# Kernel optimization log

Hardware: AMD Instinct MI355X
Metric: run time of the kernel (lower is better)

The kernel has to match this reference:

```python
import jax, jax.numpy as jnp
import numpy as np

N, M, D, E, G = 2048, 1024, 1024, 64, 16  # queries, keys, feat_dim, embed_dim, groups


def setup_inputs() -> dict:
    key = jax.random.key(0)
    ks = jax.random.split(key, 8)
    s = 0.02
    return {
        "ref_feat": jax.random.normal(ks[0], (N, D), jnp.float32),
        "sup_feat": jax.random.normal(ks[1], (M, D), jnp.float32),
        "position_embedding": jax.random.normal(ks[2], (1, E, N, M), jnp.float32),
        "fc_w": jax.random.normal(ks[3], (D, D), jnp.float32) * s,
        "fc_b": jnp.zeros((D,), jnp.float32),
        "wg_w": jax.random.normal(ks[4], (G, E, 1, 1), jnp.float32) * s,
        "wg_b": jnp.zeros((G,), jnp.float32),
        "wq_w": jax.random.normal(ks[5], (D, D), jnp.float32) * s,
        "wq_b": jnp.zeros((D,), jnp.float32),
        "wk_w": jax.random.normal(ks[6], (D, D), jnp.float32) * s,
        "wk_b": jnp.zeros((D,), jnp.float32),
        "wv_w": jax.random.normal(ks[7], (D, D, 1, 1), jnp.float32) * 0.01,
        "wv_b": jnp.zeros((D,), jnp.float32),
    }


def reference(ref_feat, sup_feat, position_embedding, fc_w, fc_b, wg_w, wg_b,
              wq_w, wq_b, wk_w, wk_b, wv_w, wv_b):
    n, d = ref_feat.shape
    g = wg_w.shape[0]
    dg = d // g  # head dim

    # shared fc (layer 0) with relu on both streams
    sup = jax.nn.relu(sup_feat @ fc_w.T + fc_b)   # [M, D]
    ref = jax.nn.relu(ref_feat @ fc_w.T + fc_b)   # [N, D]

    # position bias: 1x1 conv (E->G) + relu -> [N, G, M]
    aff_weight = jax.nn.relu(
        jnp.einsum('ge,enm->ngm', wg_w[:, :, 0, 0], position_embedding[0])
        + wg_b[None, :, None])

    # per-head q/k
    q = (ref @ wq_w.T + wq_b).reshape(n, g, dg)          # [N, G, dg]
    k = (sup @ wk_w.T + wk_b).reshape(-1, g, dg)          # [M, G, dg]

    aff_scale = jnp.einsum('ngd,mgd->ngm', q, k) / jnp.sqrt(jnp.float32(dg))
    weighted_aff = jnp.log(aff_weight + 1e-6) + aff_scale  # [N, G, M]
    aff_softmax = jax.nn.softmax(weighted_aff, axis=2)

    # value aggregation: v = sup, then grouped 1x1 conv Wv
    out_t = jnp.einsum('ngm,md->ngd', aff_softmax, sup)   # [N, G, D]
    wv = wv_w[:, :, 0, 0].reshape(g, dg, d)               # [G, D/G out, D in per group]
    attention = jnp.einsum('ngc,gjc->ngj', out_t, wv).reshape(n, d) + wv_b

    return ref + attention
```

## Files before the change

### kernel.cpp

```cpp
#include <hip/hip_runtime.h>

typedef __attribute__((ext_vector_type(8))) short short8;
typedef __attribute__((ext_vector_type(4))) float f32x4;

__device__ __forceinline__ unsigned short bf16r(float f) {
  unsigned int u = __float_as_uint(f);
  u = (u + 0x7FFFu + ((u >> 16) & 1u)) >> 16;
  return (unsigned short)u;
}
__device__ __forceinline__ float bf2f(unsigned short h) {
  return __uint_as_float(((unsigned int)h) << 16);
}
__device__ __forceinline__ unsigned int pk2(float a, float b) {
  return (unsigned int)bf16r(a) | ((unsigned int)bf16r(b) << 16);
}

__device__ __forceinline__ void gload16(const unsigned short* g, unsigned short* l) {
  __builtin_amdgcn_global_load_lds(
      (const __attribute__((address_space(1))) unsigned int*)g,
      (__attribute__((address_space(3))) unsigned int*)l, 16, 0, 0);
}

__device__ __forceinline__ void stage_tile(const unsigned short* __restrict__ gsrc, int ld,
                                           int k0, unsigned short* Ls, int t) {
  const int w = t >> 6;
  const int o0 = t * 16;
  const int r0 = o0 >> 6;
  const int c0 = ((((o0 >> 4) & 3) ^ ((r0 >> 2) & 3)) << 3);
  const int r1 = r0 + 64;
  const int c1 = ((((o0 >> 4) & 3) ^ ((r1 >> 2) & 3)) << 3);
  gload16(gsrc + (long)r0 * ld + k0 + c0, Ls + w * 512);
  gload16(gsrc + (long)r1 * ld + k0 + c1, Ls + 2048 + w * 512);
}

__device__ __forceinline__ void kloop(const unsigned short* __restrict__ A,
                                      const unsigned short* __restrict__ B,
                                      int lda, int ldb, int K,
                                      unsigned short* As, unsigned short* Bs,
                                      int t, f32x4 acc[4][4]) {
  const int lane = t & 63;
  const int w = t >> 6;
  const int wr = w >> 1, wc = w & 1;
  const int ra = lane & 15;
  const int ch = ((lane >> 4) ^ (ra >> 2)) << 3;
  stage_tile(A, lda, 0, As, t);
  stage_tile(B, ldb, 0, Bs, t);
  __syncthreads();
  for (int k0 = 0; k0 < K; k0 += 32) {
    const int p = (k0 >> 5) & 1;
    unsigned short* Ac = As + p * 4096;
    unsigned short* Bc = Bs + p * 4096;
    if (k0 + 32 < K) {
      stage_tile(A, lda, k0 + 32, As + (p ^ 1) * 4096, t);
      stage_tile(B, ldb, k0 + 32, Bs + (p ^ 1) * 4096, t);
    }
    short8 a[4], b[4];
#pragma unroll
    for (int i = 0; i < 4; ++i)
      a[i] = *(const short8*)(Ac + (wr * 64 + i * 16 + ra) * 32 + ch);
#pragma unroll
    for (int j = 0; j < 4; ++j)
      b[j] = *(const short8*)(Bc + (wc * 64 + j * 16 + ra) * 32 + ch);
#pragma unroll
    for (int i = 0; i < 4; ++i)
#pragma unroll
      for (int j = 0; j < 4; ++j)
        acc[i][j] = __builtin_amdgcn_mfma_f32_16x16x32_bf16(b[j], a[i], acc[i][j], 0, 0, 0);
    __syncthreads();
  }
}

__global__ __launch_bounds__(256)
void cvt_all(const float* __restrict__ ref, const float* __restrict__ sup,
             const float* __restrict__ fcw, const float* __restrict__ wq,
             const float* __restrict__ wk, const float* __restrict__ wv,
             unsigned short* __restrict__ Xb, unsigned short* __restrict__ FCW,
             unsigned short* __restrict__ WQB, unsigned short* __restrict__ WKB,
             unsigned short* __restrict__ WVB) {
  long u = ((long)blockIdx.x * 256 + threadIdx.x) * 4;
  const float* src; unsigned short* dst;
  if (u < 2097152)      { src = ref + u;             dst = Xb + u; }
  else if (u < 3145728) { src = sup + (u - 2097152); dst = Xb + u; }
  else if (u < 4194304) { src = fcw + (u - 3145728); dst = FCW + (u - 3145728); }
  else if (u < 5242880) { src = wq + (u - 4194304);  dst = WQB + (u - 4194304); }
  else if (u < 6291456) { src = wk + (u - 5242880);  dst = WKB + (u - 5242880); }
  else                  { src = wv + (u - 6291456);  dst = WVB + (u - 6291456); }
  float4 v = *(const float4*)src;
  ushort4 o;
  o.x = bf16r(v.x); o.y = bf16r(v.y); o.z = bf16r(v.z); o.w = bf16r(v.w);
  *(ushort4*)dst = o;
}

__global__ __launch_bounds__(256)
void gemm_fc(const unsigned short* __restrict__ X, const unsigned short* __restrict__ W,
             const float* __restrict__ bias, unsigned short* __restrict__ RS) {
  __shared__ unsigned short As[8192], Bs[8192];
  const int t = threadIdx.x, lane = t & 63, w = t >> 6;
  const int wr = w >> 1, wc = w & 1;
  const int row0 = blockIdx.x * 128, col0 = blockIdx.y * 128;
  f32x4 acc[4][4] = {};
  kloop(X + (long)row0 * 1024, W + (long)col0 * 1024, 1024, 1024, 1024, As, Bs, t, acc);
  const int rl = lane & 15, q4 = (lane >> 4) << 2;
#pragma unroll
  for (int i = 0; i < 4; ++i) {
    int rr = row0 + wr * 64 + i * 16 + rl;
#pragma unroll
    for (int j = 0; j < 4; ++j) {
      int cc = col0 + wc * 64 + j * 16 + q4;
      float4 bb = *(const float4*)(bias + cc);
      float v0 = fmaxf(acc[i][j][0] + bb.x, 0.f);
      float v1 = fmaxf(acc[i][j][1] + bb.y, 0.f);
      float v2 = fmaxf(acc[i][j][2] + bb.z, 0.f);
      float v3 = fmaxf(acc[i][j][3] + bb.w, 0.f);
      uint2 o; o.x = pk2(v0, v1); o.y = pk2(v2, v3);
      *(uint2*)(RS + (long)rr * 1024 + cc) = o;
    }
  }
}

__global__ __launch_bounds__(256)
void gemm_qkv(const unsigned short* __restrict__ RS,
              const unsigned short* __restrict__ WQ, const unsigned short* __restrict__ WK,
              const unsigned short* __restrict__ WV,
              const float* __restrict__ qb, const float* __restrict__ kb,
              unsigned short* __restrict__ QG, unsigned short* __restrict__ KG,
              unsigned short* __restrict__ SVT) {
  const int z = blockIdx.z;
  const unsigned short* A; const unsigned short* B; int M;
  if (z == 0)      { A = RS;           B = WQ; M = 2048; }
  else if (z == 1) { A = RS + 2097152; B = WK; M = 1024; }
  else             { A = RS + 2097152; B = WV; M = 1024; }
  const int row0 = blockIdx.x * 128;
  if (row0 >= M) return;
  const int col0 = blockIdx.y * 128;
  __shared__ unsigned short As[8192], Bs[8192];
  const int t = threadIdx.x, lane = t & 63, w = t >> 6;
  const int wr = w >> 1, wc = w & 1;
  f32x4 acc[4][4] = {};
  kloop(A + (long)row0 * 1024, B + (long)col0 * 1024, 1024, 1024, 1024, As, Bs, t, acc);
  const int rl = lane & 15, q4 = (lane >> 4) << 2;
  if (z == 2) {
#pragma unroll
    for (int i = 0; i < 4; ++i) {
      int rr = row0 + wr * 64 + i * 16 + rl;
#pragma unroll
      for (int j = 0; j < 4; ++j) {
        int cg = col0 + wc * 64 + j * 16 + q4;
#pragma unroll
        for (int ri = 0; ri < 4; ++ri) {
          int gg = (cg + ri) >> 6, jj = (cg + ri) & 63;
          SVT[(long)gg * 65536 + (long)jj * 1024 + rr] = bf16r(acc[i][j][ri]);
        }
      }
    }
  } else {
    const float* bias = z ? kb : qb;
    unsigned short* out = z ? KG : QG;
    const long gs = z ? 65536 : 131072;
#pragma unroll
    for (int i = 0; i < 4; ++i) {
      int rr = row0 + wr * 64 + i * 16 + rl;
#pragma unroll
      for (int j = 0; j < 4; ++j) {
        int cc = col0 + wc * 64 + j * 16 + q4;
        float4 bb = *(const float4*)(bias + cc);
        int gg = cc >> 6, jj = cc & 63;
        uint2 o;
        o.x = pk2(acc[i][j][0] + bb.x, acc[i][j][1] + bb.y);
        o.y = pk2(acc[i][j][2] + bb.z, acc[i][j][3] + bb.w);
        *(uint2*)(out + (long)gg * gs + (long)rr * 64 + jj) = o;
      }
    }
  }
}

__global__ __launch_bounds__(256)
void gemm_scores(const unsigned short* __restrict__ QG, const unsigned short* __restrict__ KG,
                 unsigned short* __restrict__ SC) {
  const int g = blockIdx.z;
  const unsigned short* A = QG + (long)g * 131072;
  const unsigned short* B = KG + (long)g * 65536;
  const int t = threadIdx.x, lane = t & 63, w = t >> 6;
  const int wr = w >> 1, wc = w & 1;
  const int row0 = blockIdx.x * 128 + wr * 64, col0 = blockIdx.y * 128 + wc * 64;
  const int ra = lane & 15, kg8 = (lane >> 4) << 3;
  f32x4 acc[4][4] = {};
#pragma unroll
  for (int k0 = 0; k0 < 64; k0 += 32) {
    short8 a[4], b[4];
#pragma unroll
    for (int i = 0; i < 4; ++i)
      a[i] = *(const short8*)(A + (long)(row0 + i * 16 + ra) * 64 + k0 + kg8);
#pragma unroll
    for (int j = 0; j < 4; ++j)
      b[j] = *(const short8*)(B + (long)(col0 + j * 16 + ra) * 64 + k0 + kg8);
#pragma unroll
    for (int i = 0; i < 4; ++i)
#pragma unroll
      for (int j = 0; j < 4; ++j)
        acc[i][j] = __builtin_amdgcn_mfma_f32_16x16x32_bf16(b[j], a[i], acc[i][j], 0, 0, 0);
  }
  const int rl = lane & 15, q4 = (lane >> 4) << 2;
  const float s = 0.18033688011112042f;
#pragma unroll
  for (int i = 0; i < 4; ++i) {
    int rr = row0 + i * 16 + rl;
#pragma unroll
    for (int j = 0; j < 4; ++j) {
      int cc = col0 + j * 16 + q4;
      uint2 o;
      o.x = pk2(acc[i][j][0] * s, acc[i][j][1] * s);
      o.y = pk2(acc[i][j][2] * s, acc[i][j][3] * s);
      *(uint2*)(SC + (long)g * 2097152 + (long)rr * 1024 + cc) = o;
    }
  }
}

__global__ __launch_bounds__(256)
void pe_softmax(const float* __restrict__ pe, const float* __restrict__ wgw,
                const float* __restrict__ wgb, unsigned short* __restrict__ Sc) {
  const int n = blockIdx.x;
  const int t = threadIdx.x;
  const int lane = t & 63;
  const int wid = t >> 6;
  __shared__ __align__(16) float wgT[64][16];
  __shared__ float redM[4][16];
  __shared__ float redS[4][16];
  for (int i = t; i < 1024; i += 256) wgT[i & 63][i >> 6] = wgw[i];
  __syncthreads();

  float acc[64];
#pragma unroll
  for (int g = 0; g < 16; ++g) {
    float bb = wgb[g];
#pragma unroll
    for (int mm = 0; mm < 4; ++mm) acc[g * 4 + mm] = bb;
  }

  const float* pebase = pe + (long)n * 1024 + t * 4;
#pragma unroll 2
  for (int e = 0; e < 64; ++e) {
    float4 p = *(const float4*)(pebase + (long)e * 2097152);
    const f32x4* wrow = (const f32x4*)(&wgT[e][0]);
    f32x4 w0 = wrow[0], w1 = wrow[1], w2 = wrow[2], w3 = wrow[3];
    float wg16[16] = {w0[0], w0[1], w0[2], w0[3], w1[0], w1[1], w1[2], w1[3],
                      w2[0], w2[1], w2[2], w2[3], w3[0], w3[1], w3[2], w3[3]};
#pragma unroll
    for (int g = 0; g < 16; ++g) {
      acc[g * 4 + 0] = fmaf(wg16[g], p.x, acc[g * 4 + 0]);
      acc[g * 4 + 1] = fmaf(wg16[g], p.y, acc[g * 4 + 1]);
      acc[g * 4 + 2] = fmaf(wg16[g], p.z, acc[g * 4 + 2]);
      acc[g * 4 + 3] = fmaf(wg16[g], p.w, acc[g * 4 + 3]);
    }
  }

#pragma unroll
  for (int g = 0; g < 16; ++g) {
    ushort4 s4 = *(const ushort4*)(Sc + (long)g * 2097152 + (long)n * 1024 + t * 4);
    acc[g * 4 + 0] = __builtin_amdgcn_logf(fmaxf(acc[g * 4 + 0], 0.f) + 1e-6f) + bf2f(s4.x);
    acc[g * 4 + 1] = __builtin_amdgcn_logf(fmaxf(acc[g * 4 + 1], 0.f) + 1e-6f) + bf2f(s4.y);
    acc[g * 4 + 2] = __builtin_amdgcn_logf(fmaxf(acc[g * 4 + 2], 0.f) + 1e-6f) + bf2f(s4.z);
    acc[g * 4 + 3] = __builtin_amdgcn_logf(fmaxf(acc[g * 4 + 3], 0.f) + 1e-6f) + bf2f(s4.w);
  }

  float gmax[16];
#pragma unroll
  for (int g = 0; g < 16; ++g) {
    float m = fmaxf(fmaxf(acc[g * 4 + 0], acc[g * 4 + 1]),
                    fmaxf(acc[g * 4 + 2], acc[g * 4 + 3]));
#pragma unroll
    for (int off = 32; off >= 1; off >>= 1) m = fmaxf(m, __shfl_xor(m, off));
    if (lane == 0) redM[wid][g] = m;
  }
  __syncthreads();
#pragma unroll
  for (int g = 0; g < 16; ++g)
    gmax[g] = fmaxf(fmaxf(redM[0][g], redM[1][g]), fmaxf(redM[2][g], redM[3][g]));

#pragma unroll
  for (int g = 0; g < 16; ++g) {
    float s = __builtin_amdgcn_exp2f(acc[g * 4 + 0] - gmax[g])
            + __builtin_amdgcn_exp2f(acc[g * 4 + 1] - gmax[g])
            + __builtin_amdgcn_exp2f(acc[g * 4 + 2] - gmax[g])
            + __builtin_amdgcn_exp2f(acc[g * 4 + 3] - gmax[g]);
#pragma unroll
    for (int off = 32; off >= 1; off >>= 1) s += __shfl_xor(s, off);
    if (lane == 0) redS[wid][g] = s;
  }
  __syncthreads();

#pragma unroll
  for (int g = 0; g < 16; ++g) {
    float sum = redS[0][g] + redS[1][g] + redS[2][g] + redS[3][g];
    float rs = __builtin_amdgcn_rcpf(sum);
    ushort4 o;
    o.x = bf16r(__builtin_amdgcn_exp2f(acc[g * 4 + 0] - gmax[g]) * rs);
    o.y = bf16r(__builtin_amdgcn_exp2f(acc[g * 4 + 1] - gmax[g]) * rs);
    o.z = bf16r(__builtin_amdgcn_exp2f(acc[g * 4 + 2] - gmax[g]) * rs);
    o.w = bf16r(__builtin_amdgcn_exp2f(acc[g * 4 + 3] - gmax[g]) * rs);
    *(ushort4*)(Sc + (long)g * 2097152 + (long)n * 1024 + t * 4) = o;
  }
}

__global__ __launch_bounds__(128)
void gemm_final(const unsigned short* __restrict__ SC, const unsigned short* __restrict__ SVT,
                const unsigned short* __restrict__ RS, const float* __restrict__ wvb,
                float* __restrict__ out) {
  const int g = blockIdx.z;
  const unsigned short* A = SC + (long)g * 2097152;
  const unsigned short* B = SVT + (long)g * 65536;
  const int t = threadIdx.x, lane = t & 63, w = t >> 6;
  const int row0 = blockIdx.x * 128 + w * 64;
  const int ra = lane & 15, kg8 = (lane >> 4) << 3;
  f32x4 acc[4][4] = {};
  short8 a0[4], b0[4], a1[4], b1[4];

#define LDF(as, bs, kk)                                                          \
  do {                                                                           \
    _Pragma("unroll") for (int i = 0; i < 4; ++i)                                \
        as[i] = *(const short8*)(A + (long)(row0 + i * 16 + ra) * 1024 + (kk) + kg8); \
    _Pragma("unroll") for (int j = 0; j < 4; ++j)                                \
        bs[j] = *(const short8*)(B + (long)(j * 16 + ra) * 1024 + (kk) + kg8);   \
  } while (0)
#define MM(as, bs)                                                               \
  do {                                                                           \
    _Pragma("unroll") for (int i = 0; i < 4; ++i)                                \
      _Pragma("unroll") for (int j = 0; j < 4; ++j)                              \
        acc[i][j] = __builtin_amdgcn_mfma_f32_16x16x32_bf16(bs[j], as[i], acc[i][j], 0, 0, 0); \
  } while (0)

  LDF(a0, b0, 0);
  for (int k0 = 0; k0 < 1024; k0 += 64) {
    LDF(a1, b1, k0 + 32);
    MM(a0, b0);
    if (k0 + 64 < 1024) LDF(a0, b0, k0 + 64);
    MM(a1, b1);
  }
#undef LDF
#undef MM

  const int rl = lane & 15, q4 = (lane >> 4) << 2;
#pragma unroll
  for (int i = 0; i < 4; ++i) {
    int rr = row0 + i * 16 + rl;
#pragma unroll
    for (int j = 0; j < 4; ++j) {
      int oc = g * 64 + j * 16 + q4;
      float4 w4 = *(const float4*)(wvb + oc);
      ushort4 r4 = *(const ushort4*)(RS + (long)rr * 1024 + oc);
      float4 o;
      o.x = acc[i][j][0] + w4.x + bf2f(r4.x);
      o.y = acc[i][j][1] + w4.y + bf2f(r4.y);
      o.z = acc[i][j][2] + w4.z + bf2f(r4.z);
      o.w = acc[i][j][3] + w4.w + bf2f(r4.w);
      *(float4*)(out + (long)rr * 1024 + oc) = o;
    }
  }
}

extern "C" void kernel_launch(void* const* d_in, const int* in_sizes, int n_in,
                              void* d_out, int out_size, void* d_ws, size_t ws_size,
                              hipStream_t stream) {
  const float* ref_feat = (const float*)d_in[0];
  const float* sup_feat = (const float*)d_in[1];
  const float* pe       = (const float*)d_in[2];
  const float* fc_w     = (const float*)d_in[3];
  const float* fc_b     = (const float*)d_in[4];
  const float* wg_w     = (const float*)d_in[5];
  const float* wg_b     = (const float*)d_in[6];
  const float* wq_w     = (const float*)d_in[7];
  const float* wq_b     = (const float*)d_in[8];
  const float* wk_w     = (const float*)d_in[9];
  const float* wk_b     = (const float*)d_in[10];
  const float* wv_w     = (const float*)d_in[11];
  const float* wv_b     = (const float*)d_in[12];

  char* ws = (char*)d_ws;
  unsigned short* Xb  = (unsigned short*)(ws);
  unsigned short* FCW = (unsigned short*)(ws + 6291456);
  unsigned short* WQB = (unsigned short*)(ws + 8388608);
  unsigned short* WKB = (unsigned short*)(ws + 10485760);
  unsigned short* WVB = (unsigned short*)(ws + 12582912);
  unsigned short* RS  = (unsigned short*)(ws + 14680064);
  unsigned short* QG  = (unsigned short*)(ws + 20971520);
  unsigned short* KG  = (unsigned short*)(ws + 25165824);
  unsigned short* SVT = (unsigned short*)(ws + 27262976);
  unsigned short* SC  = (unsigned short*)(ws + 29360128);

  cvt_all<<<7168, 256, 0, stream>>>(ref_feat, sup_feat, fc_w, wq_w, wk_w, wv_w,
                                    Xb, FCW, WQB, WKB, WVB);
  gemm_fc<<<dim3(24, 8), 256, 0, stream>>>(Xb, FCW, fc_b, RS);
  gemm_qkv<<<dim3(16, 8, 3), 256, 0, stream>>>(RS, WQB, WKB, WVB, wq_b, wk_b, QG, KG, SVT);
  gemm_scores<<<dim3(16, 8, 16), 256, 0, stream>>>(QG, KG, SC);
  pe_softmax<<<2048, 256, 0, stream>>>(pe, wg_w, wg_b, SC);
  gemm_final<<<dim3(16, 1, 16), 128, 0, stream>>>(SC, SVT, RS, wv_b, (float*)d_out);
}
```

Before: 280.2 us.

## Fuse scores, position-bias softmax and value GEMM into one flash-style kernel

Replaces the separate score GEMM, position-embedding conv plus softmax, and final value GEMM with a single kernel using online softmax over 64-key chunks. The 1x1 conv over the embedding is computed per chunk from LDS tiles loaded asynchronously into a double buffer. QK^T and PV run on MFMA inside the chunk loop. This removes the bf16 score tensor, which was written to and read back from global memory several times, and two kernel launches. In exchange, the grid is only 128 blocks of 512 threads, so the streaming read of the large embedding tensor may not keep every CU busy or saturate HBM bandwidth.

```diff
diff --git a/kernel.cpp b/kernel.cpp
--- a/kernel.cpp
+++ b/kernel.cpp
@@ -174,186 +174,171 @@
   }
 }
 
-__global__ __launch_bounds__(256)
-void gemm_scores(const unsigned short* __restrict__ QG, const unsigned short* __restrict__ KG,
-                 unsigned short* __restrict__ SC) {
-  const int g = blockIdx.z;
-  const unsigned short* A = QG + (long)g * 131072;
-  const unsigned short* B = KG + (long)g * 65536;
-  const int t = threadIdx.x, lane = t & 63, w = t >> 6;
-  const int wr = w >> 1, wc = w & 1;
-  const int row0 = blockIdx.x * 128 + wr * 64, col0 = blockIdx.y * 128 + wc * 64;
-  const int ra = lane & 15, kg8 = (lane >> 4) << 3;
-  f32x4 acc[4][4] = {};
-#pragma unroll
-  for (int k0 = 0; k0 < 64; k0 += 32) {
-    short8 a[4], b[4];
-#pragma unroll
-    for (int i = 0; i < 4; ++i)
-      a[i] = *(const short8*)(A + (long)(row0 + i * 16 + ra) * 64 + k0 + kg8);
-#pragma unroll
-    for (int j = 0; j < 4; ++j)
-      b[j] = *(const short8*)(B + (long)(col0 + j * 16 + ra) * 64 + k0 + kg8);
-#pragma unroll
-    for (int i = 0; i < 4; ++i)
-#pragma unroll
-      for (int j = 0; j < 4; ++j)
-        acc[i][j] = __builtin_amdgcn_mfma_f32_16x16x32_bf16(b[j], a[i], acc[i][j], 0, 0, 0);
-  }
-  const int rl = lane & 15, q4 = (lane >> 4) << 2;
-  const float s = 0.18033688011112042f;
-#pragma unroll
-  for (int i = 0; i < 4; ++i) {
-    int rr = row0 + i * 16 + rl;
-#pragma unroll
-    for (int j = 0; j < 4; ++j) {
-      int cc = col0 + j * 16 + q4;
-      uint2 o;
-      o.x = pk2(acc[i][j][0] * s, acc[i][j][1] * s);
-      o.y = pk2(acc[i][j][2] * s, acc[i][j][3] * s);
-      *(uint2*)(SC + (long)g * 2097152 + (long)rr * 1024 + cc) = o;
-    }
-  }
-}
-
-__global__ __launch_bounds__(256)
-void pe_softmax(const float* __restrict__ pe, const float* __restrict__ wgw,
-                const float* __restrict__ wgb, unsigned short* __restrict__ Sc) {
-  const int n = blockIdx.x;
+__global__ __launch_bounds__(512)
+void pe_attn(const float* __restrict__ pe, const float* __restrict__ wgw,
+             const float* __restrict__ wgb,
+             const unsigned short* __restrict__ QG,
+             const unsigned short* __restrict__ KG,
+             const unsigned short* __restrict__ SVT,
+             const unsigned short* __restrict__ RS,
+             const float* __restrict__ wvb, float* __restrict__ out)
+{
+  __shared__ __align__(16) unsigned char peb[2][32768];
+  __shared__ __align__(16) unsigned char Qs[32768];
+  __shared__ __align__(16) unsigned char Ps[8][2048];
+  __shared__ float wgs[1024];
+
   const int t = threadIdx.x;
   const int lane = t & 63;
-  const int wid = t >> 6;
-  __shared__ __align__(16) float wgT[64][16];
-  __shared__ float redM[4][16];
-  __shared__ float redS[4][16];
-  for (int i = t; i < 1024; i += 256) wgT[i & 63][i >> 6] = wgw[i];
-  __syncthreads();
-
-  float acc[64];
-#pragma unroll
-  for (int g = 0; g < 16; ++g) {
-    float bb = wgb[g];
-#pragma unroll
-    for (int mm = 0; mm < 4; ++mm) acc[g * 4 + mm] = bb;
-  }
-
-  const float* pebase = pe + (long)n * 1024 + t * 4;
-#pragma unroll 2
-  for (int e = 0; e < 64; ++e) {
-    float4 p = *(const float4*)(pebase + (long)e * 2097152);
-    const f32x4* wrow = (const f32x4*)(&wgT[e][0]);
-    f32x4 w0 = wrow[0], w1 = wrow[1], w2 = wrow[2], w3 = wrow[3];
-    float wg16[16] = {w0[0], w0[1], w0[2], w0[3], w1[0], w1[1], w1[2], w1[3],
-                      w2[0], w2[1], w2[2], w2[3], w3[0], w3[1], w3[2], w3[3]};
-#pragma unroll
-    for (int g = 0; g < 16; ++g) {
-      acc[g * 4 + 0] = fmaf(wg16[g], p.x, acc[g * 4 + 0]);
-      acc[g * 4 + 1] = fmaf(wg16[g], p.y, acc[g * 4 + 1]);
-      acc[g * 4 + 2] = fmaf(wg16[g], p.z, acc[g * 4 + 2]);
-      acc[g * 4 + 3] = fmaf(wg16[g], p.w, acc[g * 4 + 3]);
-    }
-  }
-
-#pragma unroll
-  for (int g = 0; g < 16; ++g) {
-    ushort4 s4 = *(const ushort4*)(Sc + (long)g * 2097152 + (long)n * 1024 + t * 4);
-    acc[g * 4 + 0] = __builtin_amdgcn_logf(fmaxf(acc[g * 4 + 0], 0.f) + 1e-6f) + bf2f(s4.x);
-    acc[g * 4 + 1] = __builtin_amdgcn_logf(fmaxf(acc[g * 4 + 1], 0.f) + 1e-6f) + bf2f(s4.y);
-    acc[g * 4 + 2] = __builtin_amdgcn_logf(fmaxf(acc[g * 4 + 2], 0.f) + 1e-6f) + bf2f(s4.z);
-    acc[g * 4 + 3] = __builtin_amdgcn_logf(fmaxf(acc[g * 4 + 3], 0.f) + 1e-6f) + bf2f(s4.w);
-  }
-
-  float gmax[16];
-#pragma unroll
-  for (int g = 0; g < 16; ++g) {
-    float m = fmaxf(fmaxf(acc[g * 4 + 0], acc[g * 4 + 1]),
-                    fmaxf(acc[g * 4 + 2], acc[g * 4 + 3]));
-#pragma unroll
-    for (int off = 32; off >= 1; off >>= 1) m = fmaxf(m, __shfl_xor(m, off));
-    if (lane == 0) redM[wid][g] = m;
-  }
-  __syncthreads();
-#pragma unroll
-  for (int g = 0; g < 16; ++g)
-    gmax[g] = fmaxf(fmaxf(redM[0][g], redM[1][g]), fmaxf(redM[2][g], redM[3][g]));
-
-#pragma unroll
-  for (int g = 0; g < 16; ++g) {
-    float s = __builtin_amdgcn_exp2f(acc[g * 4 + 0] - gmax[g])
-            + __builtin_amdgcn_exp2f(acc[g * 4 + 1] - gmax[g])
-            + __builtin_amdgcn_exp2f(acc[g * 4 + 2] - gmax[g])
-            + __builtin_amdgcn_exp2f(acc[g * 4 + 3] - gmax[g]);
-#pragma unroll
-    for (int off = 32; off >= 1; off >>= 1) s += __shfl_xor(s, off);
-    if (lane == 0) redS[wid][g] = s;
-  }
-  __syncthreads();
-
-#pragma unroll
-  for (int g = 0; g < 16; ++g) {
-    float sum = redS[0][g] + redS[1][g] + redS[2][g] + redS[3][g];
-    float rs = __builtin_amdgcn_rcpf(sum);
-    ushort4 o;
-    o.x = bf16r(__builtin_amdgcn_exp2f(acc[g * 4 + 0] - gmax[g]) * rs);
-    o.y = bf16r(__builtin_amdgcn_exp2f(acc[g * 4 + 1] - gmax[g]) * rs);
-    o.z = bf16r(__builtin_amdgcn_exp2f(acc[g * 4 + 2] - gmax[g]) * rs);
-    o.w = bf16r(__builtin_amdgcn_exp2f(acc[g * 4 + 3] - gmax[g]) * rs);
-    *(ushort4*)(Sc + (long)g * 2097152 + (long)n * 1024 + t * 4) = o;
-  }
-}
-
-__global__ __launch_bounds__(128)
-void gemm_final(const unsigned short* __restrict__ SC, const unsigned short* __restrict__ SVT,
-                const unsigned short* __restrict__ RS, const float* __restrict__ wvb,
-                float* __restrict__ out) {
-  const int g = blockIdx.z;
-  const unsigned short* A = SC + (long)g * 2097152;
-  const unsigned short* B = SVT + (long)g * 65536;
-  const int t = threadIdx.x, lane = t & 63, w = t >> 6;
-  const int row0 = blockIdx.x * 128 + w * 64;
-  const int ra = lane & 15, kg8 = (lane >> 4) << 3;
-  f32x4 acc[4][4] = {};
-  short8 a0[4], b0[4], a1[4], b1[4];
-
-#define LDF(as, bs, kk)                                                          \
-  do {                                                                           \
-    _Pragma("unroll") for (int i = 0; i < 4; ++i)                                \
-        as[i] = *(const short8*)(A + (long)(row0 + i * 16 + ra) * 1024 + (kk) + kg8); \
-    _Pragma("unroll") for (int j = 0; j < 4; ++j)                                \
-        bs[j] = *(const short8*)(B + (long)(j * 16 + ra) * 1024 + (kk) + kg8);   \
-  } while (0)
-#define MM(as, bs)                                                               \
-  do {                                                                           \
-    _Pragma("unroll") for (int i = 0; i < 4; ++i)                                \
-      _Pragma("unroll") for (int j = 0; j < 4; ++j)                              \
-        acc[i][j] = __builtin_amdgcn_mfma_f32_16x16x32_bf16(bs[j], as[i], acc[i][j], 0, 0, 0); \
-  } while (0)
-
-  LDF(a0, b0, 0);
-  for (int k0 = 0; k0 < 1024; k0 += 64) {
-    LDF(a1, b1, k0 + 32);
-    MM(a0, b0);
-    if (k0 + 64 < 1024) LDF(a0, b0, k0 + 64);
-    MM(a1, b1);
-  }
-#undef LDF
-#undef MM
-
-  const int rl = lane & 15, q4 = (lane >> 4) << 2;
-#pragma unroll
-  for (int i = 0; i < 4; ++i) {
-    int rr = row0 + i * 16 + rl;
-#pragma unroll
-    for (int j = 0; j < 4; ++j) {
-      int oc = g * 64 + j * 16 + q4;
-      float4 w4 = *(const float4*)(wvb + oc);
-      ushort4 r4 = *(const ushort4*)(RS + (long)rr * 1024 + oc);
+  const int w = t >> 6;
+  const int n0 = blockIdx.x * 16;
+  const int rl = lane & 15;
+  const int hi = lane >> 4;
+  const int g0 = w * 2;
+  const float C2 = 0.18033688011112042f;
+
+  for (int i = t; i < 1024; i += 512) wgs[(i & 63) * 16 + (i >> 6)] = wgw[i];
+  for (int u = t; u < 2048; u += 512) {
+    int r = u >> 7, rem = u & 127, g = rem >> 3, sg = rem & 7;
+    short8 q = *(const short8*)(QG + (long)g * 131072 + (long)(n0 + r) * 64 + sg * 8);
+    *(short8*)(Qs + ((r * 2048 + g * 128 + sg * 16) ^ ((r & 7) << 4))) = q;
+  }
+
+  auto STAGE = [&](int cg2) {
+    const int buf = cg2 & 1;
+    const int e = (cg2 & 7) * 8 + w;
+    const int m0s = (cg2 >> 3) * 64;
+#pragma unroll
+    for (int q = 0; q < 4; ++q) {
+      int r = 4 * q + hi;
+      int sp = (lane & 15) ^ (r & 3) ^ (((r >> 2) & 1) << 2);
+      gload16((const unsigned short*)(pe + (long)e * 2097152 + (long)(n0 + r) * 1024 + m0s + sp * 4),
+              (unsigned short*)(&peb[buf][w * 4096 + q * 1024 + lane * 16]));
+    }
+  };
+
+  STAGE(0);
+
+  f32x4 Oa[2][4] = {};
+  float mx0 = -1e30f, mx1 = -1e30f, sm0 = 0.f, sm1 = 0.f;
+  const float bias0 = wgb[g0], bias1 = wgb[g0 + 1];
+  unsigned char* Pw = Ps[w];
+  const int rowsw = rl * 256;
+  const int cmsk = ((rl & 3) << 4) ^ (((rl >> 2) & 1) << 6);
+  const int qmsk = (rl & 7) << 4;
+
+  int cg = 0;
+  for (int chunk = 0; chunk < 16; ++chunk) {
+    const int m0 = chunk * 64;
+    f32x4 conv[2][4];
+#pragma unroll
+    for (int mb = 0; mb < 4; ++mb) {
+      conv[0][mb] = (f32x4){bias0, bias0, bias0, bias0};
+      conv[1][mb] = (f32x4){bias1, bias1, bias1, bias1};
+    }
+    for (int grp = 0; grp < 8; ++grp, ++cg) {
+      __syncthreads();
+      if (cg + 1 < 128) STAGE(cg + 1);
+      const unsigned char* pb = peb[cg & 1];
+      const int ebase = (cg & 7) * 8;
+#pragma unroll
+      for (int ii = 0; ii < 8; ++ii) {
+        float wg0 = wgs[(ebase + ii) * 16 + g0];
+        float wg1 = wgs[(ebase + ii) * 16 + g0 + 1];
+#pragma unroll
+        for (int mb = 0; mb < 4; ++mb) {
+          f32x4 p = *(const f32x4*)(pb + ii * 4096 + rowsw + ((mb * 64 + hi * 16) ^ cmsk));
+          conv[0][mb] += p * wg0;
+          conv[1][mb] += p * wg1;
+        }
+      }
+    }
+    f32x4 sa[2][4];
+#pragma unroll
+    for (int gi = 0; gi < 2; ++gi) {
+      const int g = g0 + gi;
+#pragma unroll
+      for (int mb = 0; mb < 4; ++mb) {
+        f32x4 z = {};
+#pragma unroll
+        for (int kc = 0; kc < 2; ++kc) {
+          short8 kf = *(const short8*)(KG + (long)g * 65536 +
+                                       (long)(m0 + mb * 16 + rl) * 64 + kc * 32 + hi * 8);
+          short8 qf = *(const short8*)(Qs + ((rl * 2048 + g * 128 + (kc * 32 + hi * 8) * 2) ^ qmsk));
+          z = __builtin_amdgcn_mfma_f32_16x16x32_bf16(kf, qf, z, 0, 0, 0);
+        }
+        sa[gi][mb] = z;
+      }
+    }
+#pragma unroll
+    for (int gi = 0; gi < 2; ++gi) {
+      const int g = g0 + gi;
+      float wv[4][4];
+      float cmax = -1e30f;
+#pragma unroll
+      for (int mb = 0; mb < 4; ++mb)
+#pragma unroll
+        for (int ri = 0; ri < 4; ++ri) {
+          float v = __builtin_amdgcn_logf(fmaxf(conv[gi][mb][ri], 0.f) + 1e-6f)
+                  + sa[gi][mb][ri] * C2;
+          wv[mb][ri] = v;
+          cmax = fmaxf(cmax, v);
+        }
+      cmax = fmaxf(cmax, __shfl_xor(cmax, 16));
+      cmax = fmaxf(cmax, __shfl_xor(cmax, 32));
+      float oldm = gi ? mx1 : mx0;
+      float newm = fmaxf(oldm, cmax);
+      float scale = __builtin_amdgcn_exp2f(oldm - newm);
+      float csum = 0.f;
+      float pv[4][4];
+#pragma unroll
+      for (int mb = 0; mb < 4; ++mb)
+#pragma unroll
+        for (int ri = 0; ri < 4; ++ri) {
+          float p = __builtin_amdgcn_exp2f(wv[mb][ri] - newm);
+          pv[mb][ri] = p;
+          csum += p;
+        }
+      csum += __shfl_xor(csum, 16);
+      csum += __shfl_xor(csum, 32);
+      if (gi) { mx1 = newm; sm1 = sm1 * scale + csum; }
+      else    { mx0 = newm; sm0 = sm0 * scale + csum; }
+#pragma unroll
+      for (int jb = 0; jb < 4; ++jb) Oa[gi][jb] *= scale;
+#pragma unroll
+      for (int mb = 0; mb < 4; ++mb) {
+        uint2 o;
+        o.x = pk2(pv[mb][0], pv[mb][1]);
+        o.y = pk2(pv[mb][2], pv[mb][3]);
+        *(uint2*)(Pw + ((rl * 128 + mb * 32 + hi * 8) ^ qmsk)) = o;
+      }
+#pragma unroll
+      for (int jb = 0; jb < 4; ++jb) {
+#pragma unroll
+        for (int mc = 0; mc < 2; ++mc) {
+          short8 sv = *(const short8*)(SVT + (long)g * 65536 +
+                                       (long)(jb * 16 + rl) * 1024 + m0 + mc * 32 + hi * 8);
+          short8 pf = *(const short8*)(Pw + ((rl * 128 + mc * 64 + hi * 16) ^ qmsk));
+          Oa[gi][jb] = __builtin_amdgcn_mfma_f32_16x16x32_bf16(sv, pf, Oa[gi][jb], 0, 0, 0);
+        }
+      }
+    }
+  }
+  const int n = n0 + rl;
+#pragma unroll
+  for (int gi = 0; gi < 2; ++gi) {
+    float rs = __builtin_amdgcn_rcpf(gi ? sm1 : sm0);
+#pragma unroll
+    for (int jb = 0; jb < 4; ++jb) {
+      int oc = (g0 + gi) * 64 + jb * 16 + hi * 4;
+      float4 wb = *(const float4*)(wvb + oc);
+      ushort4 r4 = *(const ushort4*)(RS + (long)n * 1024 + oc);
       float4 o;
-      o.x = acc[i][j][0] + w4.x + bf2f(r4.x);
-      o.y = acc[i][j][1] + w4.y + bf2f(r4.y);
-      o.z = acc[i][j][2] + w4.z + bf2f(r4.z);
-      o.w = acc[i][j][3] + w4.w + bf2f(r4.w);
-      *(float4*)(out + (long)rr * 1024 + oc) = o;
+      o.x = Oa[gi][jb][0] * rs + wb.x + bf2f(r4.x);
+      o.y = Oa[gi][jb][1] * rs + wb.y + bf2f(r4.y);
+      o.z = Oa[gi][jb][2] * rs + wb.z + bf2f(r4.z);
+      o.w = Oa[gi][jb][3] * rs + wb.w + bf2f(r4.w);
+      *(float4*)(out + (long)n * 1024 + oc) = o;
     }
   }
 }
@@ -385,13 +370,10 @@
   unsigned short* QG  = (unsigned short*)(ws + 20971520);
   unsigned short* KG  = (unsigned short*)(ws + 25165824);
   unsigned short* SVT = (unsigned short*)(ws + 27262976);
-  unsigned short* SC  = (unsigned short*)(ws + 29360128);
 
   cvt_all<<<7168, 256, 0, stream>>>(ref_feat, sup_feat, fc_w, wq_w, wk_w, wv_w,
                                     Xb, FCW, WQB, WKB, WVB);
   gemm_fc<<<dim3(24, 8), 256, 0, stream>>>(Xb, FCW, fc_b, RS);
   gemm_qkv<<<dim3(16, 8, 3), 256, 0, stream>>>(RS, WQB, WKB, WVB, wq_b, wk_b, QG, KG, SVT);
-  gemm_scores<<<dim3(16, 8, 16), 256, 0, stream>>>(QG, KG, SC);
-  pe_softmax<<<2048, 256, 0, stream>>>(pe, wg_w, wg_b, SC);
-  gemm_final<<<dim3(16, 1, 16), 128, 0, stream>>>(SC, SVT, RS, wv_b, (float*)d_out);
-}
+  pe_attn<<<128, 512, 0, stream>>>(pe, wg_w, wg_b, QG, KG, SVT, RS, wv_b, (float*)d_out);
+}
```

After: 422.7 us. 1.51x slower.
